# Kernel optimization log

Measured on AMD Instinct MI355X. Metric: run time of the kernel, lower is better.

Reference implementation:

```python
import math
import jax, jax.numpy as jnp
import numpy as np

# gpt-oss config constants (layer_idx=1 -> sliding_window disabled)
HID = 2880
N_HEADS = 64
N_KV = 8
D_HEAD = 64
GROUPS = N_HEADS // N_KV  # 8 query heads per kv head
SLIDING_WINDOW = 0        # layer_idx % 2 == 1 -> full causal attention
SM_SCALE = 1.0 / math.sqrt(D_HEAD)
EPS = 1e-5

ROPE_BASE = 150000.0
INIT_CTX = 4096
SCALING = 32.0
NTK_ALPHA = 1.0
NTK_BETA = 32.0


def _rope_cos_sin(num_tokens: int):
    """YaRN-scaled RoPE tables, fp32, positions 0..num_tokens-1 (offset=0, no cache)."""
    d_half = D_HEAD // 2
    freq = ROPE_BASE ** (np.arange(0, D_HEAD, 2, dtype=np.float64) / D_HEAD)
    concentration = 0.1 * math.log(SCALING) + 1.0
    low = d_half * math.log(INIT_CTX / (NTK_BETA * 2 * math.pi)) / math.log(ROPE_BASE)
    high = d_half * math.log(INIT_CTX / (NTK_ALPHA * 2 * math.pi)) / math.log(ROPE_BASE)
    interpolation = 1.0 / (SCALING * freq)
    extrapolation = 1.0 / freq
    ramp = (np.arange(d_half, dtype=np.float64) - low) / (high - low)
    mask = 1.0 - np.clip(ramp, 0.0, 1.0)
    inv_freq = interpolation * (1.0 - mask) + extrapolation * mask
    t = np.arange(num_tokens, dtype=np.float64)
    freqs = np.outer(t, inv_freq)  # [S, d_half]
    cos = (np.cos(freqs) * concentration).astype(np.float32)
    sin = (np.sin(freqs) * concentration).astype(np.float32)
    return jnp.asarray(cos), jnp.asarray(sin)


def _rotate(x, cos, sin):
    # x: [B, S, nh, D]; cos/sin: [S, D/2]
    c = cos[None, :, None, :]
    s = sin[None, :, None, :]
    x1, x2 = jnp.split(x, 2, axis=-1)
    return jnp.concatenate([x1 * c - x2 * s, x2 * c + x1 * s], axis=-1)


def setup_inputs() -> dict:
    key = jax.random.key(0)
    ks = jax.random.split(key, 5)
    B, S = 1, 1536
    x = jax.random.normal(ks[0], (B, S, HID), dtype=jnp.float32)
    sinks = jax.random.normal(ks[1], (N_HEADS,), dtype=jnp.float32) * 0.5
    norm_scale = jnp.ones((HID,), dtype=jnp.float32)
    qkv_dim = D_HEAD * (N_HEADS + 2 * N_KV)  # 5120
    qkv_w = jax.random.normal(ks[2], (qkv_dim, HID), dtype=jnp.float32) * 0.02
    qkv_b = jnp.zeros((qkv_dim,), dtype=jnp.float32)
    out_w = jax.random.normal(ks[3], (HID, N_HEADS * D_HEAD), dtype=jnp.float32) * 0.02
    out_b = jnp.zeros((HID,), dtype=jnp.float32)
    return {"x": x, "sinks": sinks, "norm_scale": norm_scale,
            "qkv_w": qkv_w, "qkv_b": qkv_b, "out_w": out_w, "out_b": out_b}


def reference(x, sinks, norm_scale, qkv_w, qkv_b, out_w, out_b):
    B, S, _ = x.shape
    # RMSNorm (fp32)
    t = x * jax.lax.rsqrt(jnp.mean(x * x, axis=-1, keepdims=True) + EPS) * norm_scale
    # fused QKV projection
    qkv = jnp.einsum('bsd,od->bso', t, qkv_w) + qkv_b
    q, k, v = jnp.split(qkv, [N_HEADS * D_HEAD, (N_HEADS + N_KV) * D_HEAD], axis=-1)
    q = q.reshape(B, S, N_HEADS, D_HEAD)
    k = k.reshape(B, S, N_KV, D_HEAD)
    v = v.reshape(B, S, N_KV, D_HEAD)
    # RoPE (offset = 0, no cache)
    cos, sin = _rope_cos_sin(S)
    q = _rotate(q, cos, sin)
    k = _rotate(k, cos, sin)
    # GQA: head h = g*N_KV + kv
    q = q.reshape(B, S, GROUPS, N_KV, D_HEAD)
    scores = jnp.einsum('bqgkd,bskd->bgkqs', q, k) * SM_SCALE  # [B,G,KV,S,S]
    i = jnp.arange(S)[:, None]
    j = jnp.arange(S)[None, :]
    allowed = j <= i  # causal
    if SLIDING_WINDOW > 0:
        allowed = allowed & (i - j < SLIDING_WINDOW)
    scores = jnp.where(allowed[None, None, None, :, :], scores, -1e30)
    # softmax with learned per-head sink logit in the denominator
    sink = sinks.reshape(GROUPS, N_KV)[None, :, :, None]  # [1,G,KV,1]
    m = jnp.maximum(jnp.max(scores, axis=-1), sink)       # [B,G,KV,S]
    p = jnp.exp(scores - m[..., None])
    denom = jnp.sum(p, axis=-1) + jnp.exp(sink - m)
    attn = p / denom[..., None]
    o = jnp.einsum('bgkqs,bskd->bqgkd', attn, v).reshape(B, S, N_HEADS * D_HEAD)
    y = jnp.einsum('bse,oe->bso', o, out_w) + out_b
    return x + y
```

## Files before the change

### kernel.cpp

```cpp
#include <hip/hip_runtime.h>
#include <hip/hip_bf16.h>
#include <math.h>

typedef unsigned short u16;
typedef __attribute__((ext_vector_type(8))) short bf16x8;
typedef __attribute__((ext_vector_type(4))) float f32x4;
typedef __attribute__((ext_vector_type(4))) u16 u16x4;
typedef __attribute__((ext_vector_type(8))) u16 u16x8;

#define S_LEN   1536
#define HID     2880
#define NH      64
#define NKV     8
#define DH      64
#define QKV_N   5120
#define QDIM    4096
#define KVDIM   512
#define SMSCALE 0.125f
#define EPSV    1e-5f

__device__ __forceinline__ float b2f(u16 u) {
    unsigned int v = ((unsigned int)u) << 16;
    float f; __builtin_memcpy(&f, &v, 4); return f;
}
__device__ __forceinline__ u16 f2b(float f) {
    __hip_bfloat16 h = __float2bfloat16(f);
    return *reinterpret_cast<u16*>(&h);
}
__device__ __forceinline__ void gld16(const u16* g, u16* l) {
    __builtin_amdgcn_global_load_lds(
        (const __attribute__((address_space(1))) unsigned int*)g,
        (__attribute__((address_space(3))) unsigned int*)l, 16, 0, 0);
}
#define WAIT_VM6()   __builtin_amdgcn_s_waitcnt(0xF76)
#define WAIT_VM4()   __builtin_amdgcn_s_waitcnt(0xF74)
#define WAIT_VM0()   __builtin_amdgcn_s_waitcnt(0xF70)
#define WAIT_LGKM0() __builtin_amdgcn_s_waitcnt(0xC07F)

__global__ __launch_bounds__(256) void prep_kernel(
    const float* __restrict__ qkv_w, u16* __restrict__ qkv_w_bf,
    const float* __restrict__ x, const float* __restrict__ ns, u16* __restrict__ t,
    float* __restrict__ cosT, float* __restrict__ sinT)
{
    __shared__ float red[4];
    const int b = blockIdx.x;
    const int tid = threadIdx.x;
    if (b < 14400) {
        int i = b * 256 + tid;
        float4 v = ((const float4*)qkv_w)[i];
        u16x4 o;
        o.x = f2b(v.x); o.y = f2b(v.y); o.z = f2b(v.z); o.w = f2b(v.w);
        ((u16x4*)qkv_w_bf)[i] = o;
    } else if (b < 15936) {
        const int s = b - 14400;
        const float* xr = x + (size_t)s * HID;
        float ss = 0.f;
        for (int i = tid; i < HID; i += 256) { float v = xr[i]; ss += v * v; }
        for (int off = 32; off > 0; off >>= 1) ss += __shfl_down(ss, off);
        if ((tid & 63) == 0) red[tid >> 6] = ss;
        __syncthreads();
        float tot = red[0] + red[1] + red[2] + red[3];
        float scale = rsqrtf(tot / (float)HID + EPSV);
        u16* tr = t + (size_t)s * HID;
        for (int i = tid; i < HID; i += 256)
            tr[i] = f2b(xr[i] * scale * ns[i]);
    } else {
        int idx = (b - 15936) * 256 + tid;
        if (idx >= S_LEN * 32) return;
        int s = idx >> 5, i = idx & 31;
        const double PI2 = 6.283185307179586476925286766559;
        double base = 150000.0;
        double freq = pow(base, (double)(2 * i) / 64.0);
        double conc = 0.1 * log(32.0) + 1.0;
        double low  = 32.0 * log(4096.0 / (32.0 * PI2)) / log(base);
        double high = 32.0 * log(4096.0 / (1.0  * PI2)) / log(base);
        double interp = 1.0 / (32.0 * freq);
        double extrap = 1.0 / freq;
        double ramp = ((double)i - low) / (high - low);
        double msk = 1.0 - fmin(fmax(ramp, 0.0), 1.0);
        double invf = interp * (1.0 - msk) + extrap * msk;
        double ang = (double)s * invf;
        cosT[idx] = (float)(cos(ang) * conc);
        sinT[idx] = (float)(sin(ang) * conc);
    }
}

__global__ __launch_bounds__(256) void conv_bf16_kernel(
    const float* __restrict__ src, u16* __restrict__ dst, int n4)
{
    int i = blockIdx.x * 256 + threadIdx.x;
    if (i >= n4) return;
    float4 v = ((const float4*)src)[i];
    u16x4 o;
    o.x = f2b(v.x); o.y = f2b(v.y); o.z = f2b(v.z); o.w = f2b(v.w);
    ((u16x4*)dst)[i] = o;
}

__global__ __launch_bounds__(512, 2) void gemm_bt_8p_kernel(
    const u16* __restrict__ A, const u16* __restrict__ B,
    u16* __restrict__ Cp, u16* __restrict__ Cp2,
    int M, int N, int K, int it0, int it1, int ntm, int ntn)
{
    extern __shared__ __align__(16) u16 smem[];
    u16* sAp = smem;
    u16* sBp = smem + 32768;

    const int tid  = threadIdx.x;
    const int wave = tid >> 6, lane = tid & 63;
    const int quad = lane >> 4, l16 = lane & 15;
    const int wm = wave >> 2, wn = wave & 3;

    const int nwg  = gridDim.x;
    const int cpx  = nwg >> 3;
    const int flat = blockIdx.x;
    const int swz  = (flat & 7) * cpx + (flat >> 3);
    const int tpz  = ntm * ntn;
    const int z    = swz / tpz;
    const int rem  = swz - z * tpz;
    const int nt   = rem / ntm;
    const int mt   = rem - nt * ntm;
    const int bm = mt * 256, bn = nt * 256;
    const int niter = z ? it1 : it0;
    const int kb    = z ? (it0 + (z - 1) * it1) * 64 : 0;
    u16* C = (z < 2) ? (Cp + (size_t)z * M * N) : Cp2;

    const int r2  = tid >> 2;
    const int ks8 = (tid & 3) * 8;
    const u16* gA0 = A + (size_t)(bm + r2) * K + kb + ks8;
    const u16* gA1 = gA0 + (size_t)128 * K;
    int brA = bn + r2;       if (brA > N - 1) brA = N - 1;
    int brB = bn + 128 + r2; if (brB > N - 1) brB = N - 1;
    const u16* gB0 = B + (size_t)brA * K + kb + ks8;
    const u16* gB1 = B + (size_t)brB * K + kb + ks8;
    const int sw = wave * 512;

    f32x4 acc[8][4];
    #pragma unroll
    for (int i = 0; i < 8; i++)
        #pragma unroll
        for (int j = 0; j < 4; j++) acc[i][j] = (f32x4){0.f, 0.f, 0.f, 0.f};

    auto stA = [&](int c, int kh, int t) {
        u16* d = sAp + (((c << 1) | kh) << 13);
        const int koff = t * 64 + kh * 32;
        gld16(gA0 + koff, d + sw);
        gld16(gA1 + koff, d + 4096 + sw);
    };
    auto stB = [&](int c, int kh, int t) {
        u16* d = sBp + (((c << 1) | kh) << 13);
        const int koff = t * 64 + kh * 32;
        gld16(gB0 + koff, d + sw);
        gld16(gB1 + koff, d + 4096 + sw);
    };

    bf16x8 bv[4];
    const int arow = wm * 128 + l16;
    const int brow = wn * 64 + l16;
    auto rdB = [&](int c, int ks) {
        const u16* p = sBp + (((c << 1) | ks) << 13) + brow * 32 + quad * 8;
        #pragma unroll
        for (int nf = 0; nf < 4; nf++) bv[nf] = *(const bf16x8*)(p + nf * 16 * 32);
    };
    auto mmph = [&](int c, int ks, int mh) {
        const u16* p = sAp + (((c << 1) | ks) << 13) + (arow + mh * 64) * 32 + quad * 8;
        bf16x8 av[4];
        #pragma unroll
        for (int mf = 0; mf < 4; mf++) av[mf] = *(const bf16x8*)(p + mf * 16 * 32);
        __builtin_amdgcn_s_setprio(1);
        #pragma unroll
        for (int mf = 0; mf < 4; mf++)
            #pragma unroll
            for (int nf = 0; nf < 4; nf++)
                acc[mh * 4 + mf][nf] = __builtin_amdgcn_mfma_f32_16x16x32_bf16(
                    av[mf], bv[nf], acc[mh * 4 + mf][nf], 0, 0, 0);
        __builtin_amdgcn_s_setprio(0);
    };

    stA(0, 0, 0); stB(0, 0, 0); stA(0, 1, 0); stB(0, 1, 0);

    for (int t = 0; t < niter - 1; ++t) {
        const int c = t & 1;
        stA(c ^ 1, 0, t + 1);
        WAIT_VM6();
        __builtin_amdgcn_s_barrier();
        rdB(c, 0); mmph(c, 0, 0);
        stB(c ^ 1, 0, t + 1);
        mmph(c, 0, 1);
        stA(c ^ 1, 1, t + 1);
        WAIT_VM6();
        __builtin_amdgcn_s_barrier();
        rdB(c, 1); mmph(c, 1, 0);
        stB(c ^ 1, 1, t + 1);
        mmph(c, 1, 1);
    }
    {
        const int c = (niter - 1) & 1;
        WAIT_VM4();
        __builtin_amdgcn_s_barrier();
        rdB(c, 0); mmph(c, 0, 0); mmph(c, 0, 1);
        WAIT_VM0();
        __builtin_amdgcn_s_barrier();
        rdB(c, 1); mmph(c, 1, 0); mmph(c, 1, 1);
    }

    #pragma unroll
    for (int im = 0; im < 8; im++) {
        const int row0 = bm + wm * 128 + im * 16 + quad * 4;
        #pragma unroll
        for (int nf = 0; nf < 4; nf++) {
            const int col = bn + wn * 64 + nf * 16 + l16;
            if (col < N) {
                #pragma unroll
                for (int r = 0; r < 4; r++)
                    C[(size_t)(row0 + r) * N + col] = f2b(acc[im][nf][r]);
            }
        }
    }
}

__global__ __launch_bounds__(256) void rope_apply_kernel(
    const u16* __restrict__ p0, const u16* __restrict__ p1, const float* __restrict__ bias,
    const float* __restrict__ cosT, const float* __restrict__ sinT,
    u16* __restrict__ q_r, u16* __restrict__ k_r, u16* __restrict__ v_r)
{
    int idx = blockIdx.x * 256 + threadIdx.x;
    if (idx >= S_LEN * 320) return;
    int s = idx / 320;
    int c = idx - s * 320;
    const u16* r0p = p0 + (size_t)s * QKV_N;
    const u16* r1p = p1 + (size_t)s * QKV_N;
    if (c < 288) {
        int hh = c >> 2, j0 = (c & 3) * 8;
        int off = hh * 64;
        u16x8 a1 = *(const u16x8*)(r0p + off + j0);
        u16x8 b1 = *(const u16x8*)(r1p + off + j0);
        u16x8 a2 = *(const u16x8*)(r0p + off + 32 + j0);
        u16x8 b2 = *(const u16x8*)(r1p + off + 32 + j0);
        float bl[8], bh[8], cc[8], sn[8];
        *(float4*)&bl[0] = *(const float4*)(bias + off + j0);
        *(float4*)&bl[4] = *(const float4*)(bias + off + j0 + 4);
        *(float4*)&bh[0] = *(const float4*)(bias + off + 32 + j0);
        *(float4*)&bh[4] = *(const float4*)(bias + off + 32 + j0 + 4);
        *(float4*)&cc[0] = *(const float4*)(cosT + s * 32 + j0);
        *(float4*)&cc[4] = *(const float4*)(cosT + s * 32 + j0 + 4);
        *(float4*)&sn[0] = *(const float4*)(sinT + s * 32 + j0);
        *(float4*)&sn[4] = *(const float4*)(sinT + s * 32 + j0 + 4);
        const float scale = (hh < 64) ? SMSCALE : 1.0f;
        u16x8 lo, hi;
        #pragma unroll
        for (int j = 0; j < 8; j++) {
            float x1 = b2f(a1[j]) + b2f(b1[j]) + bl[j];
            float x2 = b2f(a2[j]) + b2f(b2[j]) + bh[j];
            lo[j] = f2b((x1 * cc[j] - x2 * sn[j]) * scale);
            hi[j] = f2b((x2 * cc[j] + x1 * sn[j]) * scale);
        }
        if (hh < 64) {
            u16* dst = q_r + (size_t)s * QDIM + off;
            *(u16x8*)(dst + j0) = lo;
            *(u16x8*)(dst + 32 + j0) = hi;
        } else {
            u16* dst = k_r + (size_t)s * KVDIM + (hh - 64) * 64;
            *(u16x8*)(dst + j0) = lo;
            *(u16x8*)(dst + 32 + j0) = hi;
        }
    } else {
        int c2 = c - 288;
        int vh = c2 >> 2, i0 = (c2 & 3) * 16;
        int off = QDIM + KVDIM + vh * 64 + i0;
        u16x8 a0 = *(const u16x8*)(r0p + off);
        u16x8 a1 = *(const u16x8*)(r0p + off + 8);
        u16x8 b0 = *(const u16x8*)(r1p + off);
        u16x8 b1 = *(const u16x8*)(r1p + off + 8);
        float bb[16];
        *(float4*)&bb[0]  = *(const float4*)(bias + off);
        *(float4*)&bb[4]  = *(const float4*)(bias + off + 4);
        *(float4*)&bb[8]  = *(const float4*)(bias + off + 8);
        *(float4*)&bb[12] = *(const float4*)(bias + off + 12);
        u16x8 o0, o1;
        #pragma unroll
        for (int j = 0; j < 8; j++) {
            o0[j] = f2b(b2f(a0[j]) + b2f(b0[j]) + bb[j]);
            o1[j] = f2b(b2f(a1[j]) + b2f(b1[j]) + bb[8 + j]);
        }
        u16* dst = v_r + (size_t)s * KVDIM + vh * 64 + i0;
        *(u16x8*)dst = o0;
        *(u16x8*)(dst + 8) = o1;
    }
}

__global__ __launch_bounds__(256) void vt_kernel(
    const u16* __restrict__ v_r, u16* __restrict__ vt)
{
    __shared__ u16 tile[64][72];
    const int s0 = blockIdx.x * 64;
    const int kvh = blockIdx.y;
    const int tid = threadIdx.x;
    const int r = tid >> 3;
    const int c = (tid & 7) * 8;

    #pragma unroll
    for (int rr = 0; rr < 64; rr += 32) {
        uint4 vv = *(const uint4*)(v_r + (size_t)(s0 + r + rr) * KVDIM + kvh * 64 + c);
        const u16* p = (const u16*)&vv;
        #pragma unroll
        for (int j = 0; j < 8; j++) tile[c + j][r + rr] = p[j];
    }
    __syncthreads();
    #pragma unroll
    for (int rr = 0; rr < 64; rr += 32) {
        uint4 ov;
        u16* p = (u16*)&ov;
        #pragma unroll
        for (int j = 0; j < 8; j++) p[j] = tile[r + rr][c + j];
        *(uint4*)(vt + (size_t)(kvh * 64 + r + rr) * S_LEN + s0 + c) = ov;
    }
}

__global__ __launch_bounds__(256) void attn_kernel(
    const u16* __restrict__ q_r, const u16* __restrict__ k_r, const u16* __restrict__ vt,
    const float* __restrict__ sinks, u16* __restrict__ o)
{
    __shared__ __align__(16) u16 sK[2][64 * 72];
    __shared__ __align__(16) u16 sVt[2][64 * 72];
    __shared__ __align__(16) u16 sP[4 * 16 * 72];

    const int bx = blockIdx.x, h = blockIdx.y;
    const int kvh = h & 7;
    const int tid = threadIdx.x, wave = tid >> 6, lane = tid & 63;
    const int quad = lane >> 4, l16 = lane & 15;
    const int srow = tid >> 3;
    const int scol = (tid & 7) * 8;
    u16* sPw = sP + wave * 16 * 72;
    const float sinkv = sinks[h];

    uint4 kreg0, kreg1, vreg0, vreg1;
    const u16* kbase = k_r + (size_t)srow * KVDIM + kvh * 64 + scol;
    const u16* vbase = vt + (size_t)(kvh * 64 + srow) * S_LEN + scol;

    auto issue = [&](int j0) {
        kreg0 = *(const uint4*)(kbase + (size_t)j0 * KVDIM);
        kreg1 = *(const uint4*)(kbase + (size_t)(j0 + 32) * KVDIM);
        vreg0 = *(const uint4*)(vbase + j0);
        vreg1 = *(const uint4*)(vbase + (size_t)32 * S_LEN + j0);
    };
    auto lwrite = [&](int c) {
        *(uint4*)(&sK[c][srow * 72 + scol])        = kreg0;
        *(uint4*)(&sK[c][(srow + 32) * 72 + scol]) = kreg1;
        *(uint4*)(&sVt[c][srow * 72 + scol])        = vreg0;
        *(uint4*)(&sVt[c][(srow + 32) * 72 + scol]) = vreg1;
    };

    for (int phase = 0; phase < 2; ++phase) {
        const int qt = phase ? (23 - bx) : bx;
        const int q_i = qt * 64 + wave * 16 + l16;
        const u16* qp = q_r + (size_t)q_i * QDIM + h * 64 + quad * 8;
        bf16x8 aq0 = *(const bf16x8*)(qp);
        bf16x8 aq1 = *(const bf16x8*)(qp + 32);

        float m_i = sinkv, l_i = 1.0f;
        f32x4 acc[4];
        #pragma unroll
        for (int dt = 0; dt < 4; dt++) acc[dt] = (f32x4){0.f, 0.f, 0.f, 0.f};

        const int ntile = qt + 1;
        issue(0);
        __syncthreads();

        for (int tt = 0; tt < ntile; ++tt) {
            const int c = tt & 1;
            lwrite(c);
            if (tt + 1 < ntile) issue((tt + 1) * 64);
            WAIT_LGKM0();
            __builtin_amdgcn_s_barrier();

            f32x4 sc[4];
            __builtin_amdgcn_s_setprio(1);
            #pragma unroll
            for (int nt = 0; nt < 4; nt++) {
                const u16* kp = &sK[c][(nt * 16 + l16) * 72 + quad * 8];
                bf16x8 bk0 = *(const bf16x8*)(kp);
                bf16x8 bk1 = *(const bf16x8*)(kp + 32);
                f32x4 s0 = (f32x4){0.f, 0.f, 0.f, 0.f};
                s0 = __builtin_amdgcn_mfma_f32_16x16x32_bf16(bk0, aq0, s0, 0, 0, 0);
                s0 = __builtin_amdgcn_mfma_f32_16x16x32_bf16(bk1, aq1, s0, 0, 0, 0);
                sc[nt] = s0;
            }
            __builtin_amdgcn_s_setprio(0);

            if (tt == qt) {
                #pragma unroll
                for (int nt = 0; nt < 4; nt++)
                    #pragma unroll
                    for (int r = 0; r < 4; r++)
                        if (tt * 64 + nt * 16 + quad * 4 + r > q_i) sc[nt][r] = -INFINITY;
            }

            float vmax = sc[0][0];
            #pragma unroll
            for (int nt = 0; nt < 4; nt++)
                #pragma unroll
                for (int r = 0; r < 4; r++) vmax = fmaxf(vmax, sc[nt][r]);
            vmax = fmaxf(vmax, __shfl_xor(vmax, 16));
            vmax = fmaxf(vmax, __shfl_xor(vmax, 32));
            if (__any(vmax > m_i + 8.0f)) {
                float mnew = fmaxf(m_i, vmax);
                float alpha = __expf(m_i - mnew);
                l_i *= alpha;
                #pragma unroll
                for (int dt = 0; dt < 4; dt++)
                    #pragma unroll
                    for (int r = 0; r < 4; r++) acc[dt][r] *= alpha;
                m_i = mnew;
            }
            float ps = 0.f;
            u16x4 pk[4];
            #pragma unroll
            for (int nt = 0; nt < 4; nt++) {
                #pragma unroll
                for (int r = 0; r < 4; r++) {
                    float p = __expf(sc[nt][r] - m_i);
                    ps += p;
                    pk[nt][r] = f2b(p);
                }
            }
            ps += __shfl_xor(ps, 16);
            ps += __shfl_xor(ps, 32);
            l_i += ps;
            #pragma unroll
            for (int nt = 0; nt < 4; nt++)
                *(u16x4*)(sPw + l16 * 72 + nt * 16 + quad * 4) = pk[nt];
            __threadfence_block();

            bf16x8 ap0 = *(const bf16x8*)(sPw + l16 * 72 + quad * 8);
            bf16x8 ap1 = *(const bf16x8*)(sPw + l16 * 72 + 32 + quad * 8);
            __builtin_amdgcn_s_setprio(1);
            #pragma unroll
            for (int dt = 0; dt < 4; dt++) {
                const u16* vp = &sVt[c][(dt * 16 + l16) * 72 + quad * 8];
                bf16x8 bv0 = *(const bf16x8*)(vp);
                bf16x8 bv1 = *(const bf16x8*)(vp + 32);
                acc[dt] = __builtin_amdgcn_mfma_f32_16x16x32_bf16(bv0, ap0, acc[dt], 0, 0, 0);
                acc[dt] = __builtin_amdgcn_mfma_f32_16x16x32_bf16(bv1, ap1, acc[dt], 0, 0, 0);
            }
            __builtin_amdgcn_s_setprio(0);
        }

        float inv = 1.0f / l_i;
        #pragma unroll
        for (int dt = 0; dt < 4; dt++) {
            u16x4 ov;
            #pragma unroll
            for (int r = 0; r < 4; r++) ov[r] = f2b(acc[dt][r] * inv);
            *(u16x4*)(o + (size_t)q_i * QDIM + h * 64 + dt * 16 + quad * 4) = ov;
        }
    }
}

__global__ __launch_bounds__(256) void final_add_kernel(
    const u16* __restrict__ p0, const u16* __restrict__ p1, const u16* __restrict__ p2,
    const float* __restrict__ bias, const float* __restrict__ x, float* __restrict__ out)
{
    int i = blockIdx.x * 256 + threadIdx.x;
    int base = i * 4;
    int col = base % HID;
    float4 xo = *(const float4*)(x + base);
    float4 bi = *(const float4*)(bias + col);
    u16x4 a = ((const u16x4*)p0)[i];
    u16x4 b = ((const u16x4*)p1)[i];
    u16x4 c = ((const u16x4*)p2)[i];
    float4 r;
    r.x = b2f(a.x) + b2f(b.x) + b2f(c.x) + bi.x + xo.x;
    r.y = b2f(a.y) + b2f(b.y) + b2f(c.y) + bi.y + xo.y;
    r.z = b2f(a.z) + b2f(b.z) + b2f(c.z) + bi.z + xo.z;
    r.w = b2f(a.w) + b2f(b.w) + b2f(c.w) + bi.w + xo.w;
    *(float4*)(out + base) = r;
}

extern "C" void kernel_launch(void* const* d_in, const int* in_sizes, int n_in,
                              void* d_out, int out_size, void* d_ws, size_t ws_size,
                              hipStream_t stream)
{
    const float* x          = (const float*)d_in[0];
    const float* sinks      = (const float*)d_in[1];
    const float* norm_scale = (const float*)d_in[2];
    const float* qkv_w      = (const float*)d_in[3];
    const float* qkv_b      = (const float*)d_in[4];
    const float* out_w      = (const float*)d_in[5];
    const float* out_b      = (const float*)d_in[6];
    float* out = (float*)d_out;

    char* ws = (char*)d_ws;
    u16* t        = (u16*)(ws);
    u16* qkv_w_bf = (u16*)(ws + 8847360);
    u16* qkvp0    = (u16*)(ws + 38338560);
    u16* qkvp1    = (u16*)(ws + 54067200);
    float* cosT   = (float*)(ws + 69795840);
    float* sinT   = (float*)(ws + 69992448);
    u16* k_r      = (u16*)(ws);
    u16* vt       = (u16*)(ws + 1572864);
    u16* q_r      = (u16*)(ws + 3145728);
    u16* o        = (u16*)(ws + 15728640);
    u16* v_r      = (u16*)(ws + 28311552);
    u16* outp0    = (u16*)(ws + 28311552);
    u16* outp1    = (u16*)(ws + 37158912);
    u16* outp2    = (u16*)(ws + 3145728);
    u16* out_w_bf = (u16*)(ws + 46006272);

    static bool lds_attr_set = false;
    if (!lds_attr_set) {
        hipFuncSetAttribute(reinterpret_cast<const void*>(gemm_bt_8p_kernel),
                            hipFuncAttributeMaxDynamicSharedMemorySize, 131072);
        lds_attr_set = true;
    }

    prep_kernel<<<16128, 256, 0, stream>>>(qkv_w, qkv_w_bf, x, norm_scale, t, cosT, sinT);
    gemm_bt_8p_kernel<<<240, 512, 131072, stream>>>(
        t, qkv_w_bf, qkvp0, qkvp0, S_LEN, QKV_N, HID, 23, 22, 6, 20);
    rope_apply_kernel<<<(S_LEN * 320) / 256, 256, 0, stream>>>(
        qkvp0, qkvp1, qkv_b, cosT, sinT, q_r, k_r, v_r);
    vt_kernel<<<dim3(S_LEN / 64, NKV), 256, 0, stream>>>(v_r, vt);
    conv_bf16_kernel<<<(HID * QDIM / 4 + 255) / 256, 256, 0, stream>>>(out_w, out_w_bf, HID * QDIM / 4);
    attn_kernel<<<dim3(12, NH), 256, 0, stream>>>(q_r, k_r, vt, sinks, o);
    gemm_bt_8p_kernel<<<216, 512, 131072, stream>>>(
        o, out_w_bf, outp0, outp2, S_LEN, HID, QDIM, 22, 21, 6, 12);
    final_add_kernel<<<S_LEN * HID / 4 / 256, 256, 0, stream>>>(outp0, outp1, outp2, out_b, x, out);
}
```

Baseline: 320.0 us.

## Halve GEMM K-step to shrink LDS and fold out_w conversion into prep

The bf16 GEMM now stages 32-wide K slices instead of 64-wide, halving dynamic LDS to 64KB, with a simpler double-buffered loop that has one barrier per iteration. Iteration counts are doubled to cover the same K range. When the workspace is large enough, the out_w fp32-to-bf16 conversion moves into the prep kernel and the separate conversion launch is dropped. The smaller LDS footprint may let more blocks share a CU. The cost is twice as many barriers and global-load issues per unit of K, with less latency hiding per stage.

```diff
diff --git a/kernel.cpp b/kernel.cpp
--- a/kernel.cpp
+++ b/kernel.cpp
@@ -32,15 +32,15 @@
         (const __attribute__((address_space(1))) unsigned int*)g,
         (__attribute__((address_space(3))) unsigned int*)l, 16, 0, 0);
 }
-#define WAIT_VM6()   __builtin_amdgcn_s_waitcnt(0xF76)
-#define WAIT_VM4()   __builtin_amdgcn_s_waitcnt(0xF74)
+#define WAIT_VM2()   __builtin_amdgcn_s_waitcnt(0xF72)
 #define WAIT_VM0()   __builtin_amdgcn_s_waitcnt(0xF70)
 #define WAIT_LGKM0() __builtin_amdgcn_s_waitcnt(0xC07F)
 
 __global__ __launch_bounds__(256) void prep_kernel(
     const float* __restrict__ qkv_w, u16* __restrict__ qkv_w_bf,
     const float* __restrict__ x, const float* __restrict__ ns, u16* __restrict__ t,
-    float* __restrict__ cosT, float* __restrict__ sinT)
+    float* __restrict__ cosT, float* __restrict__ sinT,
+    const float* __restrict__ out_w, u16* __restrict__ out_w_bf)
 {
     __shared__ float red[4];
     const int b = blockIdx.x;
@@ -64,7 +64,7 @@
         u16* tr = t + (size_t)s * HID;
         for (int i = tid; i < HID; i += 256)
             tr[i] = f2b(xr[i] * scale * ns[i]);
-    } else {
+    } else if (b < 16128) {
         int idx = (b - 15936) * 256 + tid;
         if (idx >= S_LEN * 32) return;
         int s = idx >> 5, i = idx & 31;
@@ -82,6 +82,12 @@
         double ang = (double)s * invf;
         cosT[idx] = (float)(cos(ang) * conc);
         sinT[idx] = (float)(sin(ang) * conc);
+    } else {
+        int i = (b - 16128) * 256 + tid;
+        float4 v = ((const float4*)out_w)[i];
+        u16x4 o;
+        o.x = f2b(v.x); o.y = f2b(v.y); o.z = f2b(v.z); o.w = f2b(v.w);
+        ((u16x4*)out_w_bf)[i] = o;
     }
 }
 
@@ -103,7 +109,7 @@
 {
     extern __shared__ __align__(16) u16 smem[];
     u16* sAp = smem;
-    u16* sBp = smem + 32768;
+    u16* sBp = smem + 16384;
 
     const int tid  = threadIdx.x;
     const int wave = tid >> 6, lane = tid & 63;
@@ -121,7 +127,7 @@
     const int mt   = rem - nt * ntm;
     const int bm = mt * 256, bn = nt * 256;
     const int niter = z ? it1 : it0;
-    const int kb    = z ? (it0 + (z - 1) * it1) * 64 : 0;
+    const int kb    = z ? (it0 + (z - 1) * it1) * 32 : 0;
     u16* C = (z < 2) ? (Cp + (size_t)z * M * N) : Cp2;
 
     const int r2  = tid >> 2;
@@ -140,15 +146,15 @@
         #pragma unroll
         for (int j = 0; j < 4; j++) acc[i][j] = (f32x4){0.f, 0.f, 0.f, 0.f};
 
-    auto stA = [&](int c, int kh, int t) {
-        u16* d = sAp + (((c << 1) | kh) << 13);
-        const int koff = t * 64 + kh * 32;
+    auto stA = [&](int c, int t) {
+        u16* d = sAp + c * 8192;
+        const int koff = t * 32;
         gld16(gA0 + koff, d + sw);
         gld16(gA1 + koff, d + 4096 + sw);
     };
-    auto stB = [&](int c, int kh, int t) {
-        u16* d = sBp + (((c << 1) | kh) << 13);
-        const int koff = t * 64 + kh * 32;
+    auto stB = [&](int c, int t) {
+        u16* d = sBp + c * 8192;
+        const int koff = t * 32;
         gld16(gB0 + koff, d + sw);
         gld16(gB1 + koff, d + 4096 + sw);
     };
@@ -156,13 +162,13 @@
     bf16x8 bv[4];
     const int arow = wm * 128 + l16;
     const int brow = wn * 64 + l16;
-    auto rdB = [&](int c, int ks) {
-        const u16* p = sBp + (((c << 1) | ks) << 13) + brow * 32 + quad * 8;
+    auto rdB = [&](int c) {
+        const u16* p = sBp + c * 8192 + brow * 32 + quad * 8;
         #pragma unroll
         for (int nf = 0; nf < 4; nf++) bv[nf] = *(const bf16x8*)(p + nf * 16 * 32);
     };
-    auto mmph = [&](int c, int ks, int mh) {
-        const u16* p = sAp + (((c << 1) | ks) << 13) + (arow + mh * 64) * 32 + quad * 8;
+    auto mmph = [&](int c, int mh) {
+        const u16* p = sAp + c * 8192 + (arow + mh * 64) * 32 + quad * 8;
         bf16x8 av[4];
         #pragma unroll
         for (int mf = 0; mf < 4; mf++) av[mf] = *(const bf16x8*)(p + mf * 16 * 32);
@@ -176,31 +182,25 @@
         __builtin_amdgcn_s_setprio(0);
     };
 
-    stA(0, 0, 0); stB(0, 0, 0); stA(0, 1, 0); stB(0, 1, 0);
+    stB(0, 0); stA(0, 0);
 
     for (int t = 0; t < niter - 1; ++t) {
         const int c = t & 1;
-        stA(c ^ 1, 0, t + 1);
-        WAIT_VM6();
+        stB(c ^ 1, t + 1);
+        WAIT_VM2();
         __builtin_amdgcn_s_barrier();
-        rdB(c, 0); mmph(c, 0, 0);
-        stB(c ^ 1, 0, t + 1);
-        mmph(c, 0, 1);
-        stA(c ^ 1, 1, t + 1);
-        WAIT_VM6();
-        __builtin_amdgcn_s_barrier();
-        rdB(c, 1); mmph(c, 1, 0);
-        stB(c ^ 1, 1, t + 1);
-        mmph(c, 1, 1);
+        stA(c ^ 1, t + 1);
+        rdB(c);
+        mmph(c, 0);
+        mmph(c, 1);
     }
     {
         const int c = (niter - 1) & 1;
-        WAIT_VM4();
-        __builtin_amdgcn_s_barrier();
-        rdB(c, 0); mmph(c, 0, 0); mmph(c, 0, 1);
         WAIT_VM0();
         __builtin_amdgcn_s_barrier();
-        rdB(c, 1); mmph(c, 1, 0); mmph(c, 1, 1);
+        rdB(c);
+        mmph(c, 0);
+        mmph(c, 1);
     }
 
     #pragma unroll
@@ -504,24 +504,28 @@
     u16* outp0    = (u16*)(ws + 28311552);
     u16* outp1    = (u16*)(ws + 37158912);
     u16* outp2    = (u16*)(ws + 3145728);
-    u16* out_w_bf = (u16*)(ws + 46006272);
+
+    const bool fuse_outw = (ws_size >= 93782016ull);
+    u16* out_w_bf = fuse_outw ? (u16*)(ws + 70189056) : (u16*)(ws + 46006272);
 
     static bool lds_attr_set = false;
     if (!lds_attr_set) {
         hipFuncSetAttribute(reinterpret_cast<const void*>(gemm_bt_8p_kernel),
-                            hipFuncAttributeMaxDynamicSharedMemorySize, 131072);
+                            hipFuncAttributeMaxDynamicSharedMemorySize, 65536);
         lds_attr_set = true;
     }
 
-    prep_kernel<<<16128, 256, 0, stream>>>(qkv_w, qkv_w_bf, x, norm_scale, t, cosT, sinT);
-    gemm_bt_8p_kernel<<<240, 512, 131072, stream>>>(
-        t, qkv_w_bf, qkvp0, qkvp0, S_LEN, QKV_N, HID, 23, 22, 6, 20);
+    prep_kernel<<<fuse_outw ? 27648 : 16128, 256, 0, stream>>>(
+        qkv_w, qkv_w_bf, x, norm_scale, t, cosT, sinT, out_w, out_w_bf);
+    gemm_bt_8p_kernel<<<240, 512, 65536, stream>>>(
+        t, qkv_w_bf, qkvp0, qkvp0, S_LEN, QKV_N, HID, 45, 45, 6, 20);
     rope_apply_kernel<<<(S_LEN * 320) / 256, 256, 0, stream>>>(
         qkvp0, qkvp1, qkv_b, cosT, sinT, q_r, k_r, v_r);
     vt_kernel<<<dim3(S_LEN / 64, NKV), 256, 0, stream>>>(v_r, vt);
-    conv_bf16_kernel<<<(HID * QDIM / 4 + 255) / 256, 256, 0, stream>>>(out_w, out_w_bf, HID * QDIM / 4);
+    if (!fuse_outw)
+        conv_bf16_kernel<<<(HID * QDIM / 4 + 255) / 256, 256, 0, stream>>>(out_w, out_w_bf, HID * QDIM / 4);
     attn_kernel<<<dim3(12, NH), 256, 0, stream>>>(q_r, k_r, vt, sinks, o);
-    gemm_bt_8p_kernel<<<216, 512, 131072, stream>>>(
-        o, out_w_bf, outp0, outp2, S_LEN, HID, QDIM, 22, 21, 6, 12);
+    gemm_bt_8p_kernel<<<216, 512, 65536, stream>>>(
+        o, out_w_bf, outp0, outp2, S_LEN, HID, QDIM, 44, 42, 6, 12);
     final_add_kernel<<<S_LEN * HID / 4 / 256, 256, 0, stream>>>(outp0, outp1, outp2, out_b, x, out);
 }
```

After: 309.2 us. -3.4%, faster.
